# Kernel optimization log

Hardware: AMD Instinct MI355X
Metric: run time of the kernel (lower is better)

The kernel has to match this reference:

```python
import jax, jax.numpy as jnp
import numpy as np

ALPHA = 10.0  # anchor scale: anchors = eye(C) * ALPHA


def setup_inputs() -> dict:
    key = jax.random.key(0)
    k_x, k_w = jax.random.split(key)
    B, D, C = 16384, 768, 1024
    x = jax.random.normal(k_x, (B, D), dtype=jnp.float32)
    # nn.Linear(input_dim, num_classes, bias=False).weight has shape (C, D)
    W = jax.random.normal(k_w, (C, D), dtype=jnp.float32) * (1.0 / np.sqrt(D))
    return {"x": x, "W": W}


def reference(x, W):
    # logits: (B, C) = x @ W^T
    logits = jnp.einsum("bd,cd->bc", x, W)
    # distances[b, j] = || logits[b] - alpha * e_j ||_2
    # = sqrt(||logits[b]||^2 - 2*alpha*logits[b, j] + alpha^2)
    # (exact algebraic identity for diagonal anchors; avoids the (B, C, C) intermediate)
    sq_norm = jnp.sum(logits * logits, axis=-1, keepdims=True)  # (B, 1)
    d2 = sq_norm - 2.0 * ALPHA * logits + ALPHA * ALPHA          # (B, C)
    distances = jnp.sqrt(jnp.maximum(d2, 0.0))
    return logits, distances
```

## Files before the change

### kernel.cpp

```cpp
#include <hip/hip_runtime.h>
#include <hip/hip_bf16.h>
#include <stdint.h>


#define M_DIM 16384
#define N_DIM 1024
#define K_DIM 768
#define BM 128
#define BN 128
#define BK 64
#define NT (K_DIM / BK)
#define ALPHA_F 10.0f

typedef __bf16 bf16x8 __attribute__((ext_vector_type(8)));
typedef float f32x4 __attribute__((ext_vector_type(4)));

typedef const __attribute__((address_space(1))) void* gas_ptr;
typedef __attribute__((address_space(3))) void* las_ptr;

__global__ __launch_bounds__(256) void cvt_bf16_kernel(const float* __restrict__ in,
                                                       unsigned short* __restrict__ out,
                                                       int n4) {
  int stride = gridDim.x * blockDim.x;
  for (int i = blockIdx.x * blockDim.x + threadIdx.x; i < n4; i += stride) {
    float4 v = reinterpret_cast<const float4*>(in)[i];
    union { __bf16 h[4]; ushort4 u; } p;
    p.h[0] = (__bf16)v.x;
    p.h[1] = (__bf16)v.y;
    p.h[2] = (__bf16)v.z;
    p.h[3] = (__bf16)v.w;
    reinterpret_cast<ushort4*>(out)[i] = p.u;
  }
}

__global__ __launch_bounds__(256, 2) void gemm_bf16_kernel(
    const unsigned short* __restrict__ A,
    const unsigned short* __restrict__ B,
    float* __restrict__ C) {
  __shared__ __align__(16) unsigned short lds[2][2][BM * BK];

  const int t = threadIdx.x;
  const int lane = t & 63;
  const int w = t >> 6;
  const int wr = w >> 1;
  const int wc = w & 1;

  int bid = blockIdx.x;
  int swz = (bid & 7) * 128 + (bid >> 3);
  int tn = swz & 7;
  int tm = swz >> 3;

  const unsigned short* Abase = A + (size_t)tm * BM * K_DIM;
  const unsigned short* Bbase = B + (size_t)tn * BN * K_DIM;

  f32x4 acc[4][4] = {};

  auto stage = [&](int buf, int kt) {
    const int k0 = kt * BK;
    const int row_lo = t >> 3;
    const int cs = t & 7;
#pragma unroll
    for (int i = 0; i < 4; ++i) {
      int row = i * 32 + row_lo;
      int csrc = cs ^ (row & 7);
      __builtin_amdgcn_global_load_lds(
          (gas_ptr)(const void*)(Abase + (size_t)row * K_DIM + k0 + csrc * 8),
          (las_ptr)(void*)(&lds[buf][0][0] + row * BK + cs * 8),
          16, 0, 0);
    }
#pragma unroll
    for (int i = 0; i < 4; ++i) {
      int row = i * 32 + row_lo;
      int csrc = cs ^ (row & 7);
      __builtin_amdgcn_global_load_lds(
          (gas_ptr)(const void*)(Bbase + (size_t)row * K_DIM + k0 + csrc * 8),
          (las_ptr)(void*)(&lds[buf][1][0] + row * BK + cs * 8),
          16, 0, 0);
    }
  };

  auto compute = [&](int buf) {
    const unsigned short* La = &lds[buf][0][0];
    const unsigned short* Lb = &lds[buf][1][0];
#pragma unroll
    for (int kk = 0; kk < 2; ++kk) {
      bf16x8 af[4], bfr[4];
#pragma unroll
      for (int mi = 0; mi < 4; ++mi) {
        int row = wr * 64 + mi * 16 + (lane & 15);
        int c16 = kk * 4 + (lane >> 4);
        int cs = c16 ^ (row & 7);
        af[mi] = *(const bf16x8*)(La + row * BK + cs * 8);
      }
#pragma unroll
      for (int ni = 0; ni < 4; ++ni) {
        int row = wc * 64 + ni * 16 + (lane & 15);
        int c16 = kk * 4 + (lane >> 4);
        int cs = c16 ^ (row & 7);
        bfr[ni] = *(const bf16x8*)(Lb + row * BK + cs * 8);
      }
#pragma unroll
      for (int mi = 0; mi < 4; ++mi)
#pragma unroll
        for (int ni = 0; ni < 4; ++ni)
          acc[mi][ni] = __builtin_amdgcn_mfma_f32_16x16x32_bf16(af[mi], bfr[ni], acc[mi][ni], 0, 0, 0);
    }
  };

  stage(0, 0);
  __syncthreads();
  int cur = 0;
#pragma unroll 1
  for (int kt = 0; kt < NT; ++kt) {
    if (kt + 1 < NT) stage(cur ^ 1, kt + 1);
    compute(cur);
    __syncthreads();
    cur ^= 1;
  }

  float* Cb = C + (size_t)tm * BM * N_DIM + (size_t)tn * BN;
#pragma unroll
  for (int mi = 0; mi < 4; ++mi) {
#pragma unroll
    for (int ni = 0; ni < 4; ++ni) {
      int col = wc * 64 + ni * 16 + (lane & 15);
      int row0 = wr * 64 + mi * 16 + ((lane >> 4) << 2);
      f32x4 v = acc[mi][ni];
#pragma unroll
      for (int r = 0; r < 4; ++r)
        Cb[(size_t)(row0 + r) * N_DIM + col] = v[r];
    }
  }
}

__global__ __launch_bounds__(256) void dist_kernel(const float* __restrict__ logits,
                                                   float* __restrict__ dist) {
  __shared__ float wsum[4];
  const int row = blockIdx.x;
  const int t = threadIdx.x;
  const float4* lr = reinterpret_cast<const float4*>(logits + (size_t)row * N_DIM);
  float4 v = lr[t];
  float ss = v.x * v.x + v.y * v.y + v.z * v.z + v.w * v.w;
#pragma unroll
  for (int m = 32; m >= 1; m >>= 1) ss += __shfl_xor(ss, m, 64);
  if ((t & 63) == 0) wsum[t >> 6] = ss;
  __syncthreads();
  float sq = wsum[0] + wsum[1] + wsum[2] + wsum[3];
  const float a2 = ALPHA_F * ALPHA_F;
  float4 d;
  d.x = sqrtf(fmaxf(sq - 2.0f * ALPHA_F * v.x + a2, 0.0f));
  d.y = sqrtf(fmaxf(sq - 2.0f * ALPHA_F * v.y + a2, 0.0f));
  d.z = sqrtf(fmaxf(sq - 2.0f * ALPHA_F * v.z + a2, 0.0f));
  d.w = sqrtf(fmaxf(sq - 2.0f * ALPHA_F * v.w + a2, 0.0f));
  reinterpret_cast<float4*>(dist + (size_t)row * N_DIM)[t] = d;
}

extern "C" void kernel_launch(void* const* d_in, const int* in_sizes, int n_in,
                              void* d_out, int out_size, void* d_ws, size_t ws_size,
                              hipStream_t stream) {
  const float* x = (const float*)d_in[0];
  const float* W = (const float*)d_in[1];
  float* logits = (float*)d_out;
  float* dist = logits + (size_t)M_DIM * N_DIM;

  unsigned short* xb = (unsigned short*)d_ws;
  unsigned short* Wb = xb + (size_t)M_DIM * K_DIM;

  cvt_bf16_kernel<<<2048, 256, 0, stream>>>(x, xb, M_DIM * K_DIM / 4);
  cvt_bf16_kernel<<<768, 256, 0, stream>>>(W, Wb, N_DIM * K_DIM / 4);
  gemm_bf16_kernel<<<(M_DIM / BM) * (N_DIM / BN), 256, 0, stream>>>(xb, Wb, logits);
  dist_kernel<<<M_DIM, 256, 0, stream>>>(logits, dist);
}
```

Before: 68.95 us.

## Fuse x conversion, GEMM and distance epilogue into one full-row kernel

Replaces the separate x-to-bf16 conversion, tiled GEMM and distance kernels with one kernel in which each block computes a full 64x1024 row strip. The block converts x tiles to bf16 in registers on the fly into a triple-buffered LDS ring, reads W fragments directly from global memory, reduces row sums of squares across waves through shared memory, and writes both logits and distances in the epilogue. This removes the bf16 copy of x, the extra kernel launches and the re-read of logits by the distance kernel. In exchange it uses large per-thread accumulator arrays and direct global loads of W without LDS staging, which may raise register pressure and lower occupancy.

```diff
diff --git a/kernel.cpp b/kernel.cpp
--- a/kernel.cpp
+++ b/kernel.cpp
@@ -6,153 +6,165 @@
 #define M_DIM 16384
 #define N_DIM 1024
 #define K_DIM 768
-#define BM 128
-#define BN 128
-#define BK 64
-#define NT (K_DIM / BK)
 #define ALPHA_F 10.0f
 
 typedef __bf16 bf16x8 __attribute__((ext_vector_type(8)));
 typedef float f32x4 __attribute__((ext_vector_type(4)));
 
-typedef const __attribute__((address_space(1))) void* gas_ptr;
-typedef __attribute__((address_space(3))) void* las_ptr;
+#define LGKM0 asm volatile("s_waitcnt lgkmcnt(0)" ::: "memory")
+#define PRIO1 __builtin_amdgcn_s_setprio(1)
+#define PRIO0 __builtin_amdgcn_s_setprio(0)
 
-__global__ __launch_bounds__(256) void cvt_bf16_kernel(const float* __restrict__ in,
-                                                       unsigned short* __restrict__ out,
-                                                       int n4) {
-  int stride = gridDim.x * blockDim.x;
-  for (int i = blockIdx.x * blockDim.x + threadIdx.x; i < n4; i += stride) {
-    float4 v = reinterpret_cast<const float4*>(in)[i];
-    union { __bf16 h[4]; ushort4 u; } p;
-    p.h[0] = (__bf16)v.x;
-    p.h[1] = (__bf16)v.y;
-    p.h[2] = (__bf16)v.z;
-    p.h[3] = (__bf16)v.w;
-    reinterpret_cast<ushort4*>(out)[i] = p.u;
-  }
+static __device__ __forceinline__ void bar() {
+  asm volatile("" ::: "memory");
+  __builtin_amdgcn_s_barrier();
+  asm volatile("" ::: "memory");
 }
 
-__global__ __launch_bounds__(256, 2) void gemm_bf16_kernel(
-    const unsigned short* __restrict__ A,
-    const unsigned short* __restrict__ B,
-    float* __restrict__ C) {
-  __shared__ __align__(16) unsigned short lds[2][2][BM * BK];
+__global__ __launch_bounds__(256) void cvt_w_kernel(const float* __restrict__ in,
+                                                    unsigned short* __restrict__ out) {
+  int i = blockIdx.x * 256 + threadIdx.x;
+  f32x4 v = reinterpret_cast<const f32x4*>(in)[i];
+  union { __bf16 h[4]; ushort4 u; } p;
+  p.h[0] = (__bf16)v[0]; p.h[1] = (__bf16)v[1];
+  p.h[2] = (__bf16)v[2]; p.h[3] = (__bf16)v[3];
+  reinterpret_cast<ushort4*>(out)[i] = p.u;
+}
+
+__global__ __launch_bounds__(512, 2) void fused_kernel(
+    const float* __restrict__ X,
+    const unsigned short* __restrict__ Wb,
+    float* __restrict__ logits,
+    float* __restrict__ dist) {
+  __shared__ __align__(16) unsigned short ldsA[3][64 * 64];
+  __shared__ float rs[64][8];
 
   const int t = threadIdx.x;
   const int lane = t & 63;
   const int w = t >> 6;
-  const int wr = w >> 1;
-  const int wc = w & 1;
+  const int tm = blockIdx.x;
 
-  int bid = blockIdx.x;
-  int swz = (bid & 7) * 128 + (bid >> 3);
-  int tn = swz & 7;
-  int tm = swz >> 3;
+  const float* Xb = X + (size_t)tm * 64 * K_DIM;
 
-  const unsigned short* Abase = A + (size_t)tm * BM * K_DIM;
-  const unsigned short* Bbase = B + (size_t)tn * BN * K_DIM;
+  const int srow = t >> 3, scs = t & 7;
+  const float* sgp = Xb + (size_t)srow * K_DIM + (scs ^ (srow & 7)) * 8;
 
-  f32x4 acc[4][4] = {};
+  auto cvt8 = [&](f32x4 a, f32x4 b) -> bf16x8 {
+    union { __bf16 h[8]; bf16x8 v; } p;
+    p.h[0] = (__bf16)a[0]; p.h[1] = (__bf16)a[1];
+    p.h[2] = (__bf16)a[2]; p.h[3] = (__bf16)a[3];
+    p.h[4] = (__bf16)b[0]; p.h[5] = (__bf16)b[1];
+    p.h[6] = (__bf16)b[2]; p.h[7] = (__bf16)b[3];
+    return p.v;
+  };
 
-  auto stage = [&](int buf, int kt) {
-    const int k0 = kt * BK;
-    const int row_lo = t >> 3;
-    const int cs = t & 7;
+  f32x4 acc[4][8] = {};
+
+  const unsigned short* wbase =
+      Wb + (size_t)(w * 128 + (lane & 15)) * K_DIM + (lane >> 4) * 8;
+
+  f32x4 ra0, ra1, rb0, rb1;
+
+  { const f32x4* p = (const f32x4*)(sgp + 0 * 64); ra0 = p[0]; ra1 = p[1]; }
+  { const f32x4* p = (const f32x4*)(sgp + 1 * 64); rb0 = p[0]; rb1 = p[1]; }
+  *(bf16x8*)(&ldsA[0][0] + t * 8) = cvt8(ra0, ra1);
+  *(bf16x8*)(&ldsA[1][0] + t * 8) = cvt8(rb0, rb1);
+  { const f32x4* p = (const f32x4*)(sgp + 2 * 64); ra0 = p[0]; ra1 = p[1]; }
+  { const f32x4* p = (const f32x4*)(sgp + 3 * 64); rb0 = p[0]; rb1 = p[1]; }
+  LGKM0;
+  bar();
+
 #pragma unroll
-    for (int i = 0; i < 4; ++i) {
-      int row = i * 32 + row_lo;
-      int csrc = cs ^ (row & 7);
-      __builtin_amdgcn_global_load_lds(
-          (gas_ptr)(const void*)(Abase + (size_t)row * K_DIM + k0 + csrc * 8),
-          (las_ptr)(void*)(&lds[buf][0][0] + row * BK + cs * 8),
-          16, 0, 0);
+  for (int kt = 0; kt < 12; ++kt) {
+    const unsigned short* Lbuf = &ldsA[kt % 3][0];
+    bf16x8 bq[8][2];
+    const unsigned short* wp = wbase + kt * 64;
+#pragma unroll
+    for (int ni = 0; ni < 8; ++ni) {
+      bq[ni][0] = *(const bf16x8*)(wp + (size_t)ni * 16 * K_DIM);
+      bq[ni][1] = *(const bf16x8*)(wp + (size_t)ni * 16 * K_DIM + 32);
     }
 #pragma unroll
-    for (int i = 0; i < 4; ++i) {
-      int row = i * 32 + row_lo;
-      int csrc = cs ^ (row & 7);
-      __builtin_amdgcn_global_load_lds(
-          (gas_ptr)(const void*)(Bbase + (size_t)row * K_DIM + k0 + csrc * 8),
-          (las_ptr)(void*)(&lds[buf][1][0] + row * BK + cs * 8),
-          16, 0, 0);
+    for (int mi = 0; mi < 4; ++mi) {
+      int row = mi * 16 + (lane & 15);
+      bf16x8 af0 = *(const bf16x8*)(Lbuf + row * 64 + (((lane >> 4)) ^ (row & 7)) * 8);
+      bf16x8 af1 = *(const bf16x8*)(Lbuf + row * 64 + ((4 + (lane >> 4)) ^ (row & 7)) * 8);
+      PRIO1;
+#pragma unroll
+      for (int ni = 0; ni < 8; ++ni) {
+        acc[mi][ni] = __builtin_amdgcn_mfma_f32_16x16x32_bf16(af0, bq[ni][0], acc[mi][ni], 0, 0, 0);
+        acc[mi][ni] = __builtin_amdgcn_mfma_f32_16x16x32_bf16(af1, bq[ni][1], acc[mi][ni], 0, 0, 0);
+      }
+      PRIO0;
     }
-  };
-
-  auto compute = [&](int buf) {
-    const unsigned short* La = &lds[buf][0][0];
-    const unsigned short* Lb = &lds[buf][1][0];
-#pragma unroll
-    for (int kk = 0; kk < 2; ++kk) {
-      bf16x8 af[4], bfr[4];
-#pragma unroll
-      for (int mi = 0; mi < 4; ++mi) {
-        int row = wr * 64 + mi * 16 + (lane & 15);
-        int c16 = kk * 4 + (lane >> 4);
-        int cs = c16 ^ (row & 7);
-        af[mi] = *(const bf16x8*)(La + row * BK + cs * 8);
-      }
-#pragma unroll
-      for (int ni = 0; ni < 4; ++ni) {
-        int row = wc * 64 + ni * 16 + (lane & 15);
-        int c16 = kk * 4 + (lane >> 4);
-        int cs = c16 ^ (row & 7);
-        bfr[ni] = *(const bf16x8*)(Lb + row * BK + cs * 8);
-      }
-#pragma unroll
-      for (int mi = 0; mi < 4; ++mi)
-#pragma unroll
-        for (int ni = 0; ni < 4; ++ni)
-          acc[mi][ni] = __builtin_amdgcn_mfma_f32_16x16x32_bf16(af[mi], bfr[ni], acc[mi][ni], 0, 0, 0);
+    if (kt <= 9) {
+      if ((kt & 1) == 0) *(bf16x8*)(&ldsA[(kt + 2) % 3][0] + t * 8) = cvt8(ra0, ra1);
+      else               *(bf16x8*)(&ldsA[(kt + 2) % 3][0] + t * 8) = cvt8(rb0, rb1);
     }
-  };
-
-  stage(0, 0);
-  __syncthreads();
-  int cur = 0;
-#pragma unroll 1
-  for (int kt = 0; kt < NT; ++kt) {
-    if (kt + 1 < NT) stage(cur ^ 1, kt + 1);
-    compute(cur);
-    __syncthreads();
-    cur ^= 1;
+    if (kt <= 7) {
+      const f32x4* p = (const f32x4*)(sgp + (kt + 4) * 64);
+      if ((kt & 1) == 0) { ra0 = p[0]; ra1 = p[1]; }
+      else               { rb0 = p[0]; rb1 = p[1]; }
+    }
+    LGKM0;
+    bar();
   }
 
-  float* Cb = C + (size_t)tm * BM * N_DIM + (size_t)tn * BN;
+  float part[4][4];
 #pragma unroll
-  for (int mi = 0; mi < 4; ++mi) {
+  for (int mi = 0; mi < 4; ++mi)
 #pragma unroll
-    for (int ni = 0; ni < 4; ++ni) {
-      int col = wc * 64 + ni * 16 + (lane & 15);
-      int row0 = wr * 64 + mi * 16 + ((lane >> 4) << 2);
-      f32x4 v = acc[mi][ni];
+    for (int j = 0; j < 4; ++j) {
+      float s = 0.f;
 #pragma unroll
-      for (int r = 0; r < 4; ++r)
-        Cb[(size_t)(row0 + r) * N_DIM + col] = v[r];
+      for (int ni = 0; ni < 8; ++ni) { float v = acc[mi][ni][j]; s += v * v; }
+      part[mi][j] = s;
     }
+#pragma unroll
+  for (int m = 1; m <= 8; m <<= 1)
+#pragma unroll
+    for (int mi = 0; mi < 4; ++mi)
+#pragma unroll
+      for (int j = 0; j < 4; ++j)
+        part[mi][j] += __shfl_xor(part[mi][j], m, 64);
+  if ((lane & 15) == 0) {
+    int q = lane >> 4;
+#pragma unroll
+    for (int mi = 0; mi < 4; ++mi)
+#pragma unroll
+      for (int j = 0; j < 4; ++j)
+        rs[mi * 16 + q * 4 + j][w] = part[mi][j];
   }
-}
+  __syncthreads();
 
-__global__ __launch_bounds__(256) void dist_kernel(const float* __restrict__ logits,
-                                                   float* __restrict__ dist) {
-  __shared__ float wsum[4];
-  const int row = blockIdx.x;
-  const int t = threadIdx.x;
-  const float4* lr = reinterpret_cast<const float4*>(logits + (size_t)row * N_DIM);
-  float4 v = lr[t];
-  float ss = v.x * v.x + v.y * v.y + v.z * v.z + v.w * v.w;
+  float S[4][4];
 #pragma unroll
-  for (int m = 32; m >= 1; m >>= 1) ss += __shfl_xor(ss, m, 64);
-  if ((t & 63) == 0) wsum[t >> 6] = ss;
-  __syncthreads();
-  float sq = wsum[0] + wsum[1] + wsum[2] + wsum[3];
+  for (int mi = 0; mi < 4; ++mi)
+#pragma unroll
+    for (int j = 0; j < 4; ++j) {
+      int row = mi * 16 + (lane >> 4) * 4 + j;
+      f32x4 a = *(const f32x4*)&rs[row][0];
+      f32x4 b = *(const f32x4*)&rs[row][4];
+      S[mi][j] = (a[0] + a[1] + a[2] + a[3]) + (b[0] + b[1] + b[2] + b[3]);
+    }
+
+  float* Lb = logits + (size_t)tm * 64 * N_DIM + w * 128;
+  float* Db = dist + (size_t)tm * 64 * N_DIM + w * 128;
   const float a2 = ALPHA_F * ALPHA_F;
-  float4 d;
-  d.x = sqrtf(fmaxf(sq - 2.0f * ALPHA_F * v.x + a2, 0.0f));
-  d.y = sqrtf(fmaxf(sq - 2.0f * ALPHA_F * v.y + a2, 0.0f));
-  d.z = sqrtf(fmaxf(sq - 2.0f * ALPHA_F * v.z + a2, 0.0f));
-  d.w = sqrtf(fmaxf(sq - 2.0f * ALPHA_F * v.w + a2, 0.0f));
-  reinterpret_cast<float4*>(dist + (size_t)row * N_DIM)[t] = d;
+#pragma unroll
+  for (int mi = 0; mi < 4; ++mi)
+#pragma unroll
+    for (int ni = 0; ni < 8; ++ni) {
+      int col = ni * 16 + (lane & 15);
+      int row0 = mi * 16 + ((lane >> 4) << 2);
+#pragma unroll
+      for (int r = 0; r < 4; ++r) {
+        float lv = acc[mi][ni][r];
+        Lb[(size_t)(row0 + r) * N_DIM + col] = lv;
+        float d2 = S[mi][r] - 2.0f * ALPHA_F * lv + a2;
+        Db[(size_t)(row0 + r) * N_DIM + col] = sqrtf(fmaxf(d2, 0.0f));
+      }
+    }
 }
 
 extern "C" void kernel_launch(void* const* d_in, const int* in_sizes, int n_in,
@@ -163,11 +175,8 @@
   float* logits = (float*)d_out;
   float* dist = logits + (size_t)M_DIM * N_DIM;
 
-  unsigned short* xb = (unsigned short*)d_ws;
-  unsigned short* Wb = xb + (size_t)M_DIM * K_DIM;
+  unsigned short* Wb = (unsigned short*)d_ws;
 
-  cvt_bf16_kernel<<<2048, 256, 0, stream>>>(x, xb, M_DIM * K_DIM / 4);
-  cvt_bf16_kernel<<<768, 256, 0, stream>>>(W, Wb, N_DIM * K_DIM / 4);
-  gemm_bf16_kernel<<<(M_DIM / BM) * (N_DIM / BN), 256, 0, stream>>>(xb, Wb, logits);
-  dist_kernel<<<M_DIM, 256, 0, stream>>>(logits, dist);
+  cvt_w_kernel<<<N_DIM * K_DIM / 4 / 256, 256, 0, stream>>>(W, Wb);
+  fused_kernel<<<M_DIM / 64, 512, 0, stream>>>(x, Wb, logits, dist);
 }
```

Measured after the change: 86.55 us. 25.5% more time.
